# Kernel tuning notes

Measured on AMD Instinct MI355X. Metric: run time of the kernel, lower is better.

The kernel has to match this reference:

```python
import jax, jax.numpy as jnp
import numpy as np

N = 100000
E = 3200000
NFEAT = 256
NHID = 128
NCLASS = 16
TEXT_CNT = 50000


def setup_inputs() -> dict:
    key = jax.random.key(0)
    ks = jax.random.split(key, 12)
    x = jax.random.normal(ks[0], (N, NFEAT), dtype=jnp.float32)
    adj_rows = jax.random.randint(ks[1], (E,), 0, N, dtype=jnp.int32)
    adj_cols = jax.random.randint(ks[2], (E,), 0, N, dtype=jnp.int32)
    # positive normalized-adjacency-like weights (~1/avg_degree scale)
    adj_vals = jax.random.uniform(ks[3], (E,), dtype=jnp.float32) / 32.0
    W1 = jax.random.normal(ks[4], (NFEAT, NHID), dtype=jnp.float32) / np.sqrt(NFEAT)
    b1 = jax.random.normal(ks[5], (NHID,), dtype=jnp.float32) * 0.01
    W2 = jax.random.normal(ks[6], (NHID, NFEAT), dtype=jnp.float32) / np.sqrt(NHID)
    b2 = jax.random.normal(ks[7], (NFEAT,), dtype=jnp.float32) * 0.01
    cW1 = jax.random.normal(ks[8], (NFEAT, NCLASS), dtype=jnp.float32) / np.sqrt(NFEAT)
    cb1 = jax.random.normal(ks[9], (NCLASS,), dtype=jnp.float32) * 0.01
    cW2 = jax.random.normal(ks[10], (NFEAT, NCLASS), dtype=jnp.float32) / np.sqrt(NFEAT)
    cb2 = jax.random.normal(ks[11], (NCLASS,), dtype=jnp.float32) * 0.01
    return {"x": x, "adj_rows": adj_rows, "adj_cols": adj_cols, "adj_vals": adj_vals,
            "W1": W1, "b1": b1, "W2": W2, "b2": b2,
            "cW1": cW1, "cb1": cb1, "cW2": cw2 if (cw2 := None) else cW2, "cb2": cb2}


def spmm(rows, cols, vals, dense):
    # out[r] = sum_{e: rows[e]==r} vals[e] * dense[cols[e]]   (COO SpMM)
    gathered = vals[:, None] * dense[cols]  # [E, D]
    return jax.ops.segment_sum(gathered, rows, num_segments=N)


def reference(x, adj_rows, adj_cols, adj_vals, W1, b1, W2, b2, cW1, cb1, cW2, cb2):
    # gc1: adj @ (x @ W1) + b1, then ReLU (dropout is identity at inference)
    h = jax.nn.relu(spmm(adj_rows, adj_cols, adj_vals, x @ W1) + b1)  # [N, NHID]
    # gc2: adj @ (h @ W2) + b2
    out = spmm(adj_rows, adj_cols, adj_vals, h @ W2) + b2  # [N, NFEAT]
    text_cls = out[:TEXT_CNT] @ cW1 + cb1  # [TEXT_CNT, NCLASS]
    img_cls = out[TEXT_CNT:] @ cW2 + cb2   # [N-TEXT_CNT, NCLASS]
    return (out, text_cls, img_cls)
```

## Files before the change

kernel.cpp:

```cpp
#include <hip/hip_runtime.h>

#define N_NODES  100000
#define N_EDGES  3200000
#define NFEAT    256
#define NHID     128
#define NCLASS   16
#define TEXT_CNT 50000

#define RPB      256
#define NB       ((N_NODES + RPB - 1) / RPB)
#define CAP      16384
#define S_EPT    8
#define NBLKS    ((N_EDGES + 256 * S_EPT - 1) / (256 * S_EPT))

typedef unsigned int uint;
typedef __bf16 bf16x8 __attribute__((ext_vector_type(8)));
typedef __bf16 bf16x4 __attribute__((ext_vector_type(4)));
typedef float f32x4 __attribute__((ext_vector_type(4)));

__device__ inline uint bf16_rne(float f) {
  uint u = __float_as_uint(f);
  return (u + 0x7fffu + ((u >> 16) & 1u)) >> 16;
}
__device__ inline float bf_lo(uint u) { return __uint_as_float(u << 16); }
__device__ inline float bf_hi(uint u) { return __uint_as_float(u & 0xffff0000u); }


__global__ __launch_bounds__(256) void prep_kernel(const float* __restrict__ W1,
                                                   const float* __restrict__ W2,
                                                   const float* __restrict__ b2,
                                                   const float* __restrict__ cW1,
                                                   const float* __restrict__ cb1,
                                                   const float* __restrict__ cW2,
                                                   const float* __restrict__ cb2,
                                                   unsigned short* __restrict__ W1t,
                                                   unsigned short* __restrict__ W2t,
                                                   float* __restrict__ Wc1, float* __restrict__ bc1,
                                                   float* __restrict__ Wc2, float* __restrict__ bc2,
                                                   int* __restrict__ gcursor) {
  int idx = blockIdx.x * 256 + threadIdx.x;
  if (idx < 32768) {
    int n = idx >> 8, k = idx & 255;
    W1t[idx] = (unsigned short)bf16_rne(W1[(size_t)k * NHID + n]);
  } else if (idx < 65536) {
    int i2 = idx - 32768;
    int n = i2 >> 7, k = i2 & 127;
    W2t[i2] = (unsigned short)bf16_rne(W2[(size_t)k * NFEAT + n]);
  } else if (idx < 69632) {
    int e = idx - 65536;
    int set = e >> 11;
    int e2 = e & 2047;
    int i = e2 >> 4, c = e2 & 15;
    const float* cw = set ? cW2 : cW1;
    float acc = 0.f;
    for (int k = 0; k < NFEAT; ++k)
      acc += W2[(size_t)i * NFEAT + k] * cw[k * NCLASS + c];
    (set ? Wc2 : Wc1)[e2] = acc;
    if (e < 32) {
      int s2 = e >> 4, c2 = e & 15;
      const float* cwb = s2 ? cW2 : cW1;
      float b = (s2 ? cb2 : cb1)[c2];
      for (int k = 0; k < NFEAT; ++k) b += b2[k] * cwb[k * NCLASS + c2];
      (s2 ? bc2 : bc1)[c2] = b;
    }
  } else if (idx < 69632 + NB) {
    int b = idx - 69632;
    gcursor[b] = b * CAP;
  }
}


__device__ __forceinline__ void scatter_body(int bx, const int* __restrict__ rows,
                                             const int* __restrict__ cols,
                                             const float* __restrict__ vals,
                                             int* __restrict__ gcursor,
                                             int2* __restrict__ packed, int E) {
  __shared__ int hist[NB];
  __shared__ int cur[NB];
  for (int i = threadIdx.x; i < NB; i += 256) hist[i] = 0;
  __syncthreads();
  int base = bx * (256 * S_EPT);
#pragma unroll
  for (int i = 0; i < S_EPT; ++i) {
    int e = base + i * 256 + threadIdx.x;
    if (e < E) atomicAdd(&hist[rows[e] >> 8], 1);
  }
  __syncthreads();
  for (int i = threadIdx.x; i < NB; i += 256) {
    int h = hist[i];
    cur[i] = h ? atomicAdd(&gcursor[i], h) : 0;
  }
  __syncthreads();
#pragma unroll
  for (int i = 0; i < S_EPT; ++i) {
    int e = base + i * 256 + threadIdx.x;
    if (e < E) {
      int r = rows[e];
      int b = r >> 8;
      int p = atomicAdd(&cur[b], 1);
      if (p < ((b + 1) << 14))
        packed[p] = make_int2(((r & 255) << 17) | cols[e], __float_as_int(vals[e]));
    }
  }
}


template <int A_FP32, int OUT_BF16, int K, int N>
__device__ __forceinline__ void gemm_body(int bx, int by, const void* __restrict__ Aptr,
                                          const __bf16* __restrict__ Bt,
                                          const float* __restrict__ bias,
                                          void* __restrict__ Cptr, int M) {
  __shared__ __bf16 As[128 * 40];
  __shared__ __bf16 Bs[128 * 40];
  int tid = threadIdx.x;
  int lane = tid & 63;
  int w = tid >> 6;
  int wr = w >> 1, wc = w & 1;
  int brow = bx * 128;
  int bcol = by * 128;
  int r16 = lane & 15, kb = lane >> 4;

  f32x4 acc[4][4];
#pragma unroll
  for (int m = 0; m < 4; ++m)
#pragma unroll
    for (int n = 0; n < 4; ++n) acc[m][n] = (f32x4){0.f, 0.f, 0.f, 0.f};

  for (int k0 = 0; k0 < K; k0 += 32) {
    if (A_FP32) {
      const float* A = (const float*)Aptr;
#pragma unroll
      for (int i = 0; i < 4; ++i) {
        int idx = tid + i * 256;
        int row = idx >> 3;
        int kq = (idx & 7) << 2;
        int gr = brow + row;
        float4 v = make_float4(0.f, 0.f, 0.f, 0.f);
        if (gr < M) v = *(const float4*)&A[(size_t)gr * K + k0 + kq];
        bf16x4 o;
        o[0] = (__bf16)v.x; o[1] = (__bf16)v.y; o[2] = (__bf16)v.z; o[3] = (__bf16)v.w;
        *(bf16x4*)&As[row * 40 + kq] = o;
      }
    } else {
      const __bf16* A = (const __bf16*)Aptr;
#pragma unroll
      for (int i = 0; i < 2; ++i) {
        int idx = tid + i * 256;
        int row = idx >> 2;
        int kq = (idx & 3) << 3;
        int gr = brow + row;
        bf16x8 v = {};
        if (gr < M) v = *(const bf16x8*)&A[(size_t)gr * K + k0 + kq];
        *(bf16x8*)&As[row * 40 + kq] = v;
      }
    }
#pragma unroll
    for (int i = 0; i < 2; ++i) {
      int idx = tid + i * 256;
      int col = idx >> 2;
      int kq = (idx & 3) << 3;
      bf16x8 v = *(const bf16x8*)&Bt[(size_t)(bcol + col) * K + k0 + kq];
      *(bf16x8*)&Bs[col * 40 + kq] = v;
    }
    __syncthreads();

    bf16x8 a[4], b[4];
#pragma unroll
    for (int m = 0; m < 4; ++m)
      a[m] = *(bf16x8*)&As[(wr * 64 + m * 16 + r16) * 40 + kb * 8];
#pragma unroll
    for (int n = 0; n < 4; ++n)
      b[n] = *(bf16x8*)&Bs[(wc * 64 + n * 16 + r16) * 40 + kb * 8];
#pragma unroll
    for (int m = 0; m < 4; ++m)
#pragma unroll
      for (int n = 0; n < 4; ++n)
        acc[m][n] = __builtin_amdgcn_mfma_f32_16x16x32_bf16(a[m], b[n], acc[m][n], 0, 0, 0);
    __syncthreads();
  }

  int crow0 = brow + wr * 64;
  int ccol0 = bcol + wc * 64;
#pragma unroll
  for (int n = 0; n < 4; ++n) {
    int col = ccol0 + n * 16 + r16;
    float bv = bias ? bias[col] : 0.f;
#pragma unroll
    for (int m = 0; m < 4; ++m) {
#pragma unroll
      for (int r = 0; r < 4; ++r) {
        int row = crow0 + m * 16 + kb * 4 + r;
        if (row < M) {
          float val = acc[m][n][r] + bv;
          if (OUT_BF16)
            ((unsigned short*)Cptr)[(size_t)row * N + col] = (unsigned short)bf16_rne(val);
          else
            ((float*)Cptr)[(size_t)row * N + col] = val;
        }
      }
    }
  }
}


__global__ __launch_bounds__(256) void fused_scatter_gemm1_kernel(
    const int* __restrict__ rows, const int* __restrict__ cols, const float* __restrict__ vals,
    int* __restrict__ gcursor, int2* __restrict__ packedA, int E,
    const float* __restrict__ x, const __bf16* __restrict__ W1t, uint* __restrict__ t1u, int M) {
  if (blockIdx.x < NBLKS)
    scatter_body(blockIdx.x, rows, cols, vals, gcursor, packedA, E);
  else
    gemm_body<1, 1, NFEAT, NHID>(blockIdx.x - NBLKS, 0, x, W1t, nullptr, t1u, M);
}


__global__ __launch_bounds__(512) void bucket_scan_kernel(const int* __restrict__ gcursor,
                                                          int* __restrict__ bbase) {
  __shared__ int s[512];
  int t = threadIdx.x;
  int v = (t < NB) ? (gcursor[t] - t * CAP) : 0;
  s[t] = v;
  __syncthreads();
  for (int off = 1; off < 512; off <<= 1) {
    int u = (t >= off) ? s[t - off] : 0;
    __syncthreads();
    s[t] += u;
    __syncthreads();
  }
  if (t < NB) bbase[t] = s[t] - v;
  if (t == 0) bbase[NB] = N_EDGES;
}


__global__ __launch_bounds__(512) void csr_finalize_kernel(const int* __restrict__ bbase,
                                                           const int2* __restrict__ packed_in,
                                                           int2* __restrict__ packed_out,
                                                           int* __restrict__ row_ptr) {
  __shared__ int hist[RPB];
  __shared__ int cur[RPB];
  int b = blockIdx.x;
  int s0 = b * CAP;
  int gout = bbase[b];
  int cnt = bbase[b + 1] - gout;
  int end = s0 + cnt;
  int t = threadIdx.x;
  if (t < RPB) hist[t] = 0;
  __syncthreads();
  {
    int i = s0 + t;
    for (; i + 1536 < end; i += 2048) {
      int2 a0 = packed_in[i], a1 = packed_in[i + 512];
      int2 a2 = packed_in[i + 1024], a3 = packed_in[i + 1536];
      atomicAdd(&hist[a0.x >> 17], 1);
      atomicAdd(&hist[a1.x >> 17], 1);
      atomicAdd(&hist[a2.x >> 17], 1);
      atomicAdd(&hist[a3.x >> 17], 1);
    }
    for (; i < end; i += 512) atomicAdd(&hist[packed_in[i].x >> 17], 1);
  }
  __syncthreads();
  int v = (t < RPB) ? hist[t] : 0;
  if (t < RPB) cur[t] = v;
  __syncthreads();
  for (int off = 1; off < RPB; off <<= 1) {
    int u = (t >= off && t < RPB) ? cur[t - off] : 0;
    __syncthreads();
    if (t < RPB) cur[t] += u;
    __syncthreads();
  }
  if (t < RPB) {
    int rbase = gout + cur[t] - v;
    int row = b * RPB + t;
    if (row < N_NODES) row_ptr[row] = rbase;
    cur[t] = rbase;
  }
  if (b == 0 && t == 0) row_ptr[N_NODES] = N_EDGES;
  __syncthreads();
  {
    int i = s0 + t;
    for (; i + 1536 < end; i += 2048) {
      int2 a0 = packed_in[i], a1 = packed_in[i + 512];
      int2 a2 = packed_in[i + 1024], a3 = packed_in[i + 1536];
      int p0 = atomicAdd(&cur[a0.x >> 17], 1);
      int p1 = atomicAdd(&cur[a1.x >> 17], 1);
      int p2 = atomicAdd(&cur[a2.x >> 17], 1);
      int p3 = atomicAdd(&cur[a3.x >> 17], 1);
      packed_out[p0] = make_int2((a0.x & 0x1FFFF) << 8, a0.y);
      packed_out[p1] = make_int2((a1.x & 0x1FFFF) << 8, a1.y);
      packed_out[p2] = make_int2((a2.x & 0x1FFFF) << 8, a2.y);
      packed_out[p3] = make_int2((a3.x & 0x1FFFF) << 8, a3.y);
    }
    for (; i < end; i += 512) {
      int2 pk = packed_in[i];
      int p = atomicAdd(&cur[pk.x >> 17], 1);
      packed_out[p] = make_int2((pk.x & 0x1FFFF) << 8, pk.y);
    }
  }
}


__global__ __launch_bounds__(256) void spmm_bf16_kernel(const int* __restrict__ row_ptr,
                                                        const int2* __restrict__ packed,
                                                        const uint* __restrict__ src,
                                                        uint* __restrict__ dst,
                                                        const float* __restrict__ bias,
                                                        int relu, int nrows) {
  int tid = threadIdx.x;
  int lane = tid & 63;
  int half = lane >> 5;
  int l32 = lane & 31;
  int row = blockIdx.x * 4 + (tid >> 6);
  if (row >= nrows) return;
  int s = row_ptr[row];
  int e = row_ptr[row + 1];
  const char* srcb = (const char*)src + (l32 << 3);
  float a0 = 0.f, a1 = 0.f, a2 = 0.f, a3 = 0.f;
  int i = s;
  for (; i + 16 <= e; i += 16) {
    int2 m0 = packed[i + 0 + half], m1 = packed[i + 2 + half];
    int2 m2 = packed[i + 4 + half], m3 = packed[i + 6 + half];
    int2 m4 = packed[i + 8 + half], m5 = packed[i + 10 + half];
    int2 m6 = packed[i + 12 + half], m7 = packed[i + 14 + half];
    uint2 u0 = *(const uint2*)(srcb + (uint)m0.x);
    uint2 u1 = *(const uint2*)(srcb + (uint)m1.x);
    uint2 u2 = *(const uint2*)(srcb + (uint)m2.x);
    uint2 u3 = *(const uint2*)(srcb + (uint)m3.x);
    uint2 u4 = *(const uint2*)(srcb + (uint)m4.x);
    uint2 u5 = *(const uint2*)(srcb + (uint)m5.x);
    uint2 u6 = *(const uint2*)(srcb + (uint)m6.x);
    uint2 u7 = *(const uint2*)(srcb + (uint)m7.x);
    float v0 = __int_as_float(m0.y), v1 = __int_as_float(m1.y);
    float v2 = __int_as_float(m2.y), v3 = __int_as_float(m3.y);
    float v4 = __int_as_float(m4.y), v5 = __int_as_float(m5.y);
    float v6 = __int_as_float(m6.y), v7 = __int_as_float(m7.y);
    a0 += v0 * bf_lo(u0.x); a1 += v0 * bf_hi(u0.x); a2 += v0 * bf_lo(u0.y); a3 += v0 * bf_hi(u0.y);
    a0 += v1 * bf_lo(u1.x); a1 += v1 * bf_hi(u1.x); a2 += v1 * bf_lo(u1.y); a3 += v1 * bf_hi(u1.y);
    a0 += v2 * bf_lo(u2.x); a1 += v2 * bf_hi(u2.x); a2 += v2 * bf_lo(u2.y); a3 += v2 * bf_hi(u2.y);
    a0 += v3 * bf_lo(u3.x); a1 += v3 * bf_hi(u3.x); a2 += v3 * bf_lo(u3.y); a3 += v3 * bf_hi(u3.y);
    a0 += v4 * bf_lo(u4.x); a1 += v4 * bf_hi(u4.x); a2 += v4 * bf_lo(u4.y); a3 += v4 * bf_hi(u4.y);
    a0 += v5 * bf_lo(u5.x); a1 += v5 * bf_hi(u5.x); a2 += v5 * bf_lo(u5.y); a3 += v5 * bf_hi(u5.y);
    a0 += v6 * bf_lo(u6.x); a1 += v6 * bf_hi(u6.x); a2 += v6 * bf_lo(u6.y); a3 += v6 * bf_hi(u6.y);
    a0 += v7 * bf_lo(u7.x); a1 += v7 * bf_hi(u7.x); a2 += v7 * bf_lo(u7.y); a3 += v7 * bf_hi(u7.y);
  }
  for (; i + 8 <= e; i += 8) {
    int2 m0 = packed[i + 0 + half], m1 = packed[i + 2 + half];
    int2 m2 = packed[i + 4 + half], m3 = packed[i + 6 + half];
    uint2 u0 = *(const uint2*)(srcb + (uint)m0.x);
    uint2 u1 = *(const uint2*)(srcb + (uint)m1.x);
    uint2 u2 = *(const uint2*)(srcb + (uint)m2.x);
    uint2 u3 = *(const uint2*)(srcb + (uint)m3.x);
    float v0 = __int_as_float(m0.y), v1 = __int_as_float(m1.y);
    float v2 = __int_as_float(m2.y), v3 = __int_as_float(m3.y);
    a0 += v0 * bf_lo(u0.x); a1 += v0 * bf_hi(u0.x); a2 += v0 * bf_lo(u0.y); a3 += v0 * bf_hi(u0.y);
    a0 += v1 * bf_lo(u1.x); a1 += v1 * bf_hi(u1.x); a2 += v1 * bf_lo(u1.y); a3 += v1 * bf_hi(u1.y);
    a0 += v2 * bf_lo(u2.x); a1 += v2 * bf_hi(u2.x); a2 += v2 * bf_lo(u2.y); a3 += v2 * bf_hi(u2.y);
    a0 += v3 * bf_lo(u3.x); a1 += v3 * bf_hi(u3.x); a2 += v3 * bf_lo(u3.y); a3 += v3 * bf_hi(u3.y);
  }
  for (; i + 4 <= e; i += 4) {
    int2 m0 = packed[i + 0 + half], m1 = packed[i + 2 + half];
    uint2 u0 = *(const uint2*)(srcb + (uint)m0.x);
    uint2 u1 = *(const uint2*)(srcb + (uint)m1.x);
    float v0 = __int_as_float(m0.y), v1 = __int_as_float(m1.y);
    a0 += v0 * bf_lo(u0.x); a1 += v0 * bf_hi(u0.x); a2 += v0 * bf_lo(u0.y); a3 += v0 * bf_hi(u0.y);
    a0 += v1 * bf_lo(u1.x); a1 += v1 * bf_hi(u1.x); a2 += v1 * bf_lo(u1.y); a3 += v1 * bf_hi(u1.y);
  }
  for (; i < e; i += 2) {
    int ee = i + half;
    int ok = ee < e;
    int2 m = packed[ok ? ee : (e - 1)];
    uint2 u = *(const uint2*)(srcb + (uint)m.x);
    float v = ok ? __int_as_float(m.y) : 0.f;
    a0 += v * bf_lo(u.x); a1 += v * bf_hi(u.x); a2 += v * bf_lo(u.y); a3 += v * bf_hi(u.y);
  }
  a0 += __shfl_xor(a0, 32); a1 += __shfl_xor(a1, 32);
  a2 += __shfl_xor(a2, 32); a3 += __shfl_xor(a3, 32);
  if (half == 0) {
    if (bias) {
      a0 += bias[4 * l32 + 0]; a1 += bias[4 * l32 + 1];
      a2 += bias[4 * l32 + 2]; a3 += bias[4 * l32 + 3];
    }
    if (relu) {
      a0 = fmaxf(a0, 0.f); a1 = fmaxf(a1, 0.f);
      a2 = fmaxf(a2, 0.f); a3 = fmaxf(a3, 0.f);
    }
    uint2 o;
    o.x = bf16_rne(a0) | (bf16_rne(a1) << 16);
    o.y = bf16_rne(a2) | (bf16_rne(a3) << 16);
    *(uint2*)&dst[(size_t)row * 64 + l32 * 2] = o;
  }
}


template <int A_FP32, int OUT_BF16, int K, int N>
__global__ __launch_bounds__(256) void gemm_mfma_kernel(const void* __restrict__ Aptr,
                                                        const __bf16* __restrict__ Bt,
                                                        const float* __restrict__ bias,
                                                        void* __restrict__ Cptr, int M) {
  gemm_body<A_FP32, OUT_BF16, K, N>(blockIdx.x, blockIdx.y, Aptr, Bt, bias, Cptr, M);
}


__global__ __launch_bounds__(256) void cls_kernel(const uint* __restrict__ t3,
                                                  const float* __restrict__ Wc1,
                                                  const float* __restrict__ bc1,
                                                  const float* __restrict__ Wc2,
                                                  const float* __restrict__ bc2,
                                                  float* __restrict__ out1,
                                                  float* __restrict__ out2) {
  int half = gridDim.x >> 1;
  int region = blockIdx.x >= half;
  int bid = region ? blockIdx.x - half : blockIdx.x;
  const float* Wc = region ? Wc2 : Wc1;
  const float* bc = region ? bc2 : bc1;
  float* outp = region ? out2 : out1;
  int row0 = region ? TEXT_CNT : 0;
  int nrows = region ? (N_NODES - TEXT_CNT) : TEXT_CNT;

  int lane = threadIdx.x & 63;
  int wav = bid * 4 + (threadIdx.x >> 6);
  int nw = half * 4;
  int c = lane & 15;
  int kg = lane >> 4;
  float w[32];
#pragma unroll
  for (int j = 0; j < 32; ++j) w[j] = Wc[(kg * 32 + j) * NCLASS + c];
  float bcv = bc[c];
  for (int r = wav; r < nrows; r += nw) {
    const uint4* rp = (const uint4*)&t3[(size_t)(row0 + r) * 64 + kg * 16];
    float acc = 0.f;
#pragma unroll
    for (int q = 0; q < 4; ++q) {
      uint4 u = rp[q];
      acc += bf_lo(u.x) * w[q * 8 + 0] + bf_hi(u.x) * w[q * 8 + 1]
           + bf_lo(u.y) * w[q * 8 + 2] + bf_hi(u.y) * w[q * 8 + 3]
           + bf_lo(u.z) * w[q * 8 + 4] + bf_hi(u.z) * w[q * 8 + 5]
           + bf_lo(u.w) * w[q * 8 + 6] + bf_hi(u.w) * w[q * 8 + 7];
    }
    acc += __shfl_xor(acc, 16);
    acc += __shfl_xor(acc, 32);
    if (lane < 16) outp[(size_t)r * NCLASS + lane] = acc + bcv;
  }
}


extern "C" void kernel_launch(void* const* d_in, const int* in_sizes, int n_in,
                              void* d_out, int out_size, void* d_ws, size_t ws_size,
                              hipStream_t stream) {
  const float* x     = (const float*)d_in[0];
  const int*   arows = (const int*)d_in[1];
  const int*   acols = (const int*)d_in[2];
  const float* avals = (const float*)d_in[3];
  const float* W1    = (const float*)d_in[4];
  const float* b1    = (const float*)d_in[5];
  const float* W2    = (const float*)d_in[6];
  const float* b2    = (const float*)d_in[7];
  const float* cW1   = (const float*)d_in[8];
  const float* cb1   = (const float*)d_in[9];
  const float* cW2   = (const float*)d_in[10];
  const float* cb2   = (const float*)d_in[11];
  float* outp = (float*)d_out;

  char* ws = (char*)d_ws;
  size_t off = 0;
  auto alloc = [&](size_t bytes) -> void* {
    void* p = ws + off;
    off += (bytes + 255) & ~(size_t)255;
    return p;
  };
  uint*  t1u     = (uint*) alloc((size_t)N_NODES * 64 * 4);
  uint*  hu      = (uint*) alloc((size_t)N_NODES * 64 * 4);
  uint*  t3u     = (uint*) alloc((size_t)N_NODES * 64 * 4);
  int2*  packedA = (int2*) alloc((size_t)NB * CAP * 8);
  int2*  packedB = (int2*) alloc((size_t)N_EDGES * 8);
  int*   bbase   = (int*)  alloc((size_t)(NB + 1) * 4);
  int*   gcursor = (int*)  alloc((size_t)NB * 4);
  int*   rowp    = (int*)  alloc((size_t)(N_NODES + 1) * 4);
  unsigned short* W1t = (unsigned short*)alloc((size_t)NHID * NFEAT * 2);
  unsigned short* W2t = (unsigned short*)alloc((size_t)NFEAT * NHID * 2);
  float* Wc1     = (float*)alloc(NHID * NCLASS * 4);
  float* Wc2     = (float*)alloc(NHID * NCLASS * 4);
  float* bc1     = (float*)alloc(64);
  float* bc2     = (float*)alloc(64);

  prep_kernel<<<(69632 + NB + 255) / 256, 256, 0, stream>>>(
      W1, W2, b2, cW1, cb1, cW2, cb2, W1t, W2t, Wc1, bc1, Wc2, bc2, gcursor);

  int mblk = (N_NODES + 127) / 128;
  fused_scatter_gemm1_kernel<<<NBLKS + mblk, 256, 0, stream>>>(
      arows, acols, avals, gcursor, packedA, N_EDGES,
      x, (const __bf16*)W1t, t1u, N_NODES);

  bucket_scan_kernel<<<1, 512, 0, stream>>>(gcursor, bbase);
  csr_finalize_kernel<<<NB, 512, 0, stream>>>(bbase, packedA, packedB, rowp);

  spmm_bf16_kernel<<<(N_NODES + 3) / 4, 256, 0, stream>>>(rowp, packedB, t1u, hu, b1, 1, N_NODES);
  spmm_bf16_kernel<<<(N_NODES + 3) / 4, 256, 0, stream>>>(rowp, packedB, hu, t3u, nullptr, 0, N_NODES);
  gemm_mfma_kernel<0, 0, NHID, NFEAT><<<dim3(mblk, 2), 256, 0, stream>>>(
      t3u, (const __bf16*)W2t, b2, outp, N_NODES);
  cls_kernel<<<2048, 256, 0, stream>>>(t3u, Wc1, bc1, Wc2, bc2,
      outp + (size_t)N_NODES * NFEAT,
      outp + (size_t)N_NODES * NFEAT + (size_t)TEXT_CNT * NCLASS);
}
```

Before: 465.3 us.

## Unfuse scatter from GEMM1, add nontemporal streaming loads, enlarge scatter per-thread work

Splits the fused scatter+GEMM1 kernel back into a standalone bucket scatter kernel and a separate GEMM1 launch that runs after CSR finalize. The scatter now handles 32 edges per thread instead of 8, and streaming reads of edge arrays, packed COO/CSR entries, x, and the final fp32 output store switch to nontemporal loads and stores. The aim is to keep the reused feature tables cached during the gathers and to cut atomic traffic on the global cursors. The cost is that the scatter no longer overlaps with GEMM1, there is one more launch, and fewer scatter blocks means less parallelism.

```diff
diff --git a/kernel.cpp b/kernel.cpp
--- a/kernel.cpp
+++ b/kernel.cpp
@@ -10,13 +10,14 @@
 #define RPB      256
 #define NB       ((N_NODES + RPB - 1) / RPB)
 #define CAP      16384
-#define S_EPT    8
+#define S_EPT    32
 #define NBLKS    ((N_EDGES + 256 * S_EPT - 1) / (256 * S_EPT))
 
 typedef unsigned int uint;
 typedef __bf16 bf16x8 __attribute__((ext_vector_type(8)));
 typedef __bf16 bf16x4 __attribute__((ext_vector_type(4)));
 typedef float f32x4 __attribute__((ext_vector_type(4)));
+typedef int i32x2 __attribute__((ext_vector_type(2)));
 
 __device__ inline uint bf16_rne(float f) {
   uint u = __float_as_uint(f);
@@ -70,20 +71,20 @@
 }
 
 
-__device__ __forceinline__ void scatter_body(int bx, const int* __restrict__ rows,
-                                             const int* __restrict__ cols,
-                                             const float* __restrict__ vals,
-                                             int* __restrict__ gcursor,
-                                             int2* __restrict__ packed, int E) {
+__global__ __launch_bounds__(256) void bucket_scatter_kernel(const int* __restrict__ rows,
+                                                             const int* __restrict__ cols,
+                                                             const float* __restrict__ vals,
+                                                             int* __restrict__ gcursor,
+                                                             int2* __restrict__ packed, int E) {
   __shared__ int hist[NB];
   __shared__ int cur[NB];
   for (int i = threadIdx.x; i < NB; i += 256) hist[i] = 0;
   __syncthreads();
-  int base = bx * (256 * S_EPT);
+  int base = blockIdx.x * (256 * S_EPT);
 #pragma unroll
   for (int i = 0; i < S_EPT; ++i) {
     int e = base + i * 256 + threadIdx.x;
-    if (e < E) atomicAdd(&hist[rows[e] >> 8], 1);
+    if (e < E) atomicAdd(&hist[__builtin_nontemporal_load(&rows[e]) >> 8], 1);
   }
   __syncthreads();
   for (int i = threadIdx.x; i < NB; i += 256) {
@@ -95,122 +96,15 @@
   for (int i = 0; i < S_EPT; ++i) {
     int e = base + i * 256 + threadIdx.x;
     if (e < E) {
-      int r = rows[e];
+      int r = __builtin_nontemporal_load(&rows[e]);
+      int c = __builtin_nontemporal_load(&cols[e]);
+      float v = __builtin_nontemporal_load(&vals[e]);
       int b = r >> 8;
       int p = atomicAdd(&cur[b], 1);
       if (p < ((b + 1) << 14))
-        packed[p] = make_int2(((r & 255) << 17) | cols[e], __float_as_int(vals[e]));
-    }
-  }
-}
-
-
-template <int A_FP32, int OUT_BF16, int K, int N>
-__device__ __forceinline__ void gemm_body(int bx, int by, const void* __restrict__ Aptr,
-                                          const __bf16* __restrict__ Bt,
-                                          const float* __restrict__ bias,
-                                          void* __restrict__ Cptr, int M) {
-  __shared__ __bf16 As[128 * 40];
-  __shared__ __bf16 Bs[128 * 40];
-  int tid = threadIdx.x;
-  int lane = tid & 63;
-  int w = tid >> 6;
-  int wr = w >> 1, wc = w & 1;
-  int brow = bx * 128;
-  int bcol = by * 128;
-  int r16 = lane & 15, kb = lane >> 4;
-
-  f32x4 acc[4][4];
-#pragma unroll
-  for (int m = 0; m < 4; ++m)
-#pragma unroll
-    for (int n = 0; n < 4; ++n) acc[m][n] = (f32x4){0.f, 0.f, 0.f, 0.f};
-
-  for (int k0 = 0; k0 < K; k0 += 32) {
-    if (A_FP32) {
-      const float* A = (const float*)Aptr;
-#pragma unroll
-      for (int i = 0; i < 4; ++i) {
-        int idx = tid + i * 256;
-        int row = idx >> 3;
-        int kq = (idx & 7) << 2;
-        int gr = brow + row;
-        float4 v = make_float4(0.f, 0.f, 0.f, 0.f);
-        if (gr < M) v = *(const float4*)&A[(size_t)gr * K + k0 + kq];
-        bf16x4 o;
-        o[0] = (__bf16)v.x; o[1] = (__bf16)v.y; o[2] = (__bf16)v.z; o[3] = (__bf16)v.w;
-        *(bf16x4*)&As[row * 40 + kq] = o;
-      }
-    } else {
-      const __bf16* A = (const __bf16*)Aptr;
-#pragma unroll
-      for (int i = 0; i < 2; ++i) {
-        int idx = tid + i * 256;
-        int row = idx >> 2;
-        int kq = (idx & 3) << 3;
-        int gr = brow + row;
-        bf16x8 v = {};
-        if (gr < M) v = *(const bf16x8*)&A[(size_t)gr * K + k0 + kq];
-        *(bf16x8*)&As[row * 40 + kq] = v;
-      }
-    }
-#pragma unroll
-    for (int i = 0; i < 2; ++i) {
-      int idx = tid + i * 256;
-      int col = idx >> 2;
-      int kq = (idx & 3) << 3;
-      bf16x8 v = *(const bf16x8*)&Bt[(size_t)(bcol + col) * K + k0 + kq];
-      *(bf16x8*)&Bs[col * 40 + kq] = v;
-    }
-    __syncthreads();
-
-    bf16x8 a[4], b[4];
-#pragma unroll
-    for (int m = 0; m < 4; ++m)
-      a[m] = *(bf16x8*)&As[(wr * 64 + m * 16 + r16) * 40 + kb * 8];
-#pragma unroll
-    for (int n = 0; n < 4; ++n)
-      b[n] = *(bf16x8*)&Bs[(wc * 64 + n * 16 + r16) * 40 + kb * 8];
-#pragma unroll
-    for (int m = 0; m < 4; ++m)
-#pragma unroll
-      for (int n = 0; n < 4; ++n)
-        acc[m][n] = __builtin_amdgcn_mfma_f32_16x16x32_bf16(a[m], b[n], acc[m][n], 0, 0, 0);
-    __syncthreads();
-  }
-
-  int crow0 = brow + wr * 64;
-  int ccol0 = bcol + wc * 64;
-#pragma unroll
-  for (int n = 0; n < 4; ++n) {
-    int col = ccol0 + n * 16 + r16;
-    float bv = bias ? bias[col] : 0.f;
-#pragma unroll
-    for (int m = 0; m < 4; ++m) {
-#pragma unroll
-      for (int r = 0; r < 4; ++r) {
-        int row = crow0 + m * 16 + kb * 4 + r;
-        if (row < M) {
-          float val = acc[m][n][r] + bv;
-          if (OUT_BF16)
-            ((unsigned short*)Cptr)[(size_t)row * N + col] = (unsigned short)bf16_rne(val);
-          else
-            ((float*)Cptr)[(size_t)row * N + col] = val;
-        }
-      }
-    }
-  }
-}
-
-
-__global__ __launch_bounds__(256) void fused_scatter_gemm1_kernel(
-    const int* __restrict__ rows, const int* __restrict__ cols, const float* __restrict__ vals,
-    int* __restrict__ gcursor, int2* __restrict__ packedA, int E,
-    const float* __restrict__ x, const __bf16* __restrict__ W1t, uint* __restrict__ t1u, int M) {
-  if (blockIdx.x < NBLKS)
-    scatter_body(blockIdx.x, rows, cols, vals, gcursor, packedA, E);
-  else
-    gemm_body<1, 1, NFEAT, NHID>(blockIdx.x - NBLKS, 0, x, W1t, nullptr, t1u, M);
+        packed[p] = make_int2(((r & 255) << 17) | c, __float_as_int(v));
+    }
+  }
 }
 
 
@@ -244,19 +138,22 @@
   int cnt = bbase[b + 1] - gout;
   int end = s0 + cnt;
   int t = threadIdx.x;
+  const i32x2* pin = (const i32x2*)packed_in;
   if (t < RPB) hist[t] = 0;
   __syncthreads();
   {
     int i = s0 + t;
     for (; i + 1536 < end; i += 2048) {
-      int2 a0 = packed_in[i], a1 = packed_in[i + 512];
-      int2 a2 = packed_in[i + 1024], a3 = packed_in[i + 1536];
+      i32x2 a0 = __builtin_nontemporal_load(&pin[i]);
+      i32x2 a1 = __builtin_nontemporal_load(&pin[i + 512]);
+      i32x2 a2 = __builtin_nontemporal_load(&pin[i + 1024]);
+      i32x2 a3 = __builtin_nontemporal_load(&pin[i + 1536]);
       atomicAdd(&hist[a0.x >> 17], 1);
       atomicAdd(&hist[a1.x >> 17], 1);
       atomicAdd(&hist[a2.x >> 17], 1);
       atomicAdd(&hist[a3.x >> 17], 1);
     }
-    for (; i < end; i += 512) atomicAdd(&hist[packed_in[i].x >> 17], 1);
+    for (; i < end; i += 512) atomicAdd(&hist[__builtin_nontemporal_load(&pin[i]).x >> 17], 1);
   }
   __syncthreads();
   int v = (t < RPB) ? hist[t] : 0;
@@ -279,8 +176,10 @@
   {
     int i = s0 + t;
     for (; i + 1536 < end; i += 2048) {
-      int2 a0 = packed_in[i], a1 = packed_in[i + 512];
-      int2 a2 = packed_in[i + 1024], a3 = packed_in[i + 1536];
+      i32x2 a0 = __builtin_nontemporal_load(&pin[i]);
+      i32x2 a1 = __builtin_nontemporal_load(&pin[i + 512]);
+      i32x2 a2 = __builtin_nontemporal_load(&pin[i + 1024]);
+      i32x2 a3 = __builtin_nontemporal_load(&pin[i + 1536]);
       int p0 = atomicAdd(&cur[a0.x >> 17], 1);
       int p1 = atomicAdd(&cur[a1.x >> 17], 1);
       int p2 = atomicAdd(&cur[a2.x >> 17], 1);
@@ -291,7 +190,7 @@
       packed_out[p3] = make_int2((a3.x & 0x1FFFF) << 8, a3.y);
     }
     for (; i < end; i += 512) {
-      int2 pk = packed_in[i];
+      i32x2 pk = __builtin_nontemporal_load(&pin[i]);
       int p = atomicAdd(&cur[pk.x >> 17], 1);
       packed_out[p] = make_int2((pk.x & 0x1FFFF) << 8, pk.y);
     }
@@ -314,13 +213,18 @@
   int s = row_ptr[row];
   int e = row_ptr[row + 1];
   const char* srcb = (const char*)src + (l32 << 3);
+  const i32x2* pk = (const i32x2*)packed;
   float a0 = 0.f, a1 = 0.f, a2 = 0.f, a3 = 0.f;
   int i = s;
   for (; i + 16 <= e; i += 16) {
-    int2 m0 = packed[i + 0 + half], m1 = packed[i + 2 + half];
-    int2 m2 = packed[i + 4 + half], m3 = packed[i + 6 + half];
-    int2 m4 = packed[i + 8 + half], m5 = packed[i + 10 + half];
-    int2 m6 = packed[i + 12 + half], m7 = packed[i + 14 + half];
+    i32x2 m0 = __builtin_nontemporal_load(&pk[i + 0 + half]);
+    i32x2 m1 = __builtin_nontemporal_load(&pk[i + 2 + half]);
+    i32x2 m2 = __builtin_nontemporal_load(&pk[i + 4 + half]);
+    i32x2 m3 = __builtin_nontemporal_load(&pk[i + 6 + half]);
+    i32x2 m4 = __builtin_nontemporal_load(&pk[i + 8 + half]);
+    i32x2 m5 = __builtin_nontemporal_load(&pk[i + 10 + half]);
+    i32x2 m6 = __builtin_nontemporal_load(&pk[i + 12 + half]);
+    i32x2 m7 = __builtin_nontemporal_load(&pk[i + 14 + half]);
     uint2 u0 = *(const uint2*)(srcb + (uint)m0.x);
     uint2 u1 = *(const uint2*)(srcb + (uint)m1.x);
     uint2 u2 = *(const uint2*)(srcb + (uint)m2.x);
@@ -343,8 +247,10 @@
     a0 += v7 * bf_lo(u7.x); a1 += v7 * bf_hi(u7.x); a2 += v7 * bf_lo(u7.y); a3 += v7 * bf_hi(u7.y);
   }
   for (; i + 8 <= e; i += 8) {
-    int2 m0 = packed[i + 0 + half], m1 = packed[i + 2 + half];
-    int2 m2 = packed[i + 4 + half], m3 = packed[i + 6 + half];
+    i32x2 m0 = __builtin_nontemporal_load(&pk[i + 0 + half]);
+    i32x2 m1 = __builtin_nontemporal_load(&pk[i + 2 + half]);
+    i32x2 m2 = __builtin_nontemporal_load(&pk[i + 4 + half]);
+    i32x2 m3 = __builtin_nontemporal_load(&pk[i + 6 + half]);
     uint2 u0 = *(const uint2*)(srcb + (uint)m0.x);
     uint2 u1 = *(const uint2*)(srcb + (uint)m1.x);
     uint2 u2 = *(const uint2*)(srcb + (uint)m2.x);
@@ -357,7 +263,8 @@
     a0 += v3 * bf_lo(u3.x); a1 += v3 * bf_hi(u3.x); a2 += v3 * bf_lo(u3.y); a3 += v3 * bf_hi(u3.y);
   }
   for (; i + 4 <= e; i += 4) {
-    int2 m0 = packed[i + 0 + half], m1 = packed[i + 2 + half];
+    i32x2 m0 = __builtin_nontemporal_load(&pk[i + 0 + half]);
+    i32x2 m1 = __builtin_nontemporal_load(&pk[i + 2 + half]);
     uint2 u0 = *(const uint2*)(srcb + (uint)m0.x);
     uint2 u1 = *(const uint2*)(srcb + (uint)m1.x);
     float v0 = __int_as_float(m0.y), v1 = __int_as_float(m1.y);
@@ -367,7 +274,7 @@
   for (; i < e; i += 2) {
     int ee = i + half;
     int ok = ee < e;
-    int2 m = packed[ok ? ee : (e - 1)];
+    i32x2 m = pk[ok ? ee : (e - 1)];
     uint2 u = *(const uint2*)(srcb + (uint)m.x);
     float v = ok ? __int_as_float(m.y) : 0.f;
     a0 += v * bf_lo(u.x); a1 += v * bf_hi(u.x); a2 += v * bf_lo(u.y); a3 += v * bf_hi(u.y);
@@ -396,7 +303,96 @@
                                                         const __bf16* __restrict__ Bt,
                                                         const float* __restrict__ bias,
                                                         void* __restrict__ Cptr, int M) {
-  gemm_body<A_FP32, OUT_BF16, K, N>(blockIdx.x, blockIdx.y, Aptr, Bt, bias, Cptr, M);
+  __shared__ __bf16 As[128 * 40];
+  __shared__ __bf16 Bs[128 * 40];
+  int tid = threadIdx.x;
+  int lane = tid & 63;
+  int w = tid >> 6;
+  int wr = w >> 1, wc = w & 1;
+  int brow = blockIdx.x * 128;
+  int bcol = blockIdx.y * 128;
+  int r16 = lane & 15, kb = lane >> 4;
+
+  f32x4 acc[4][4];
+#pragma unroll
+  for (int m = 0; m < 4; ++m)
+#pragma unroll
+    for (int n = 0; n < 4; ++n) acc[m][n] = (f32x4){0.f, 0.f, 0.f, 0.f};
+
+  for (int k0 = 0; k0 < K; k0 += 32) {
+    if (A_FP32) {
+      const float* A = (const float*)Aptr;
+#pragma unroll
+      for (int i = 0; i < 4; ++i) {
+        int idx = tid + i * 256;
+        int row = idx >> 3;
+        int kq = (idx & 7) << 2;
+        int gr = brow + row;
+        f32x4 v = (f32x4){0.f, 0.f, 0.f, 0.f};
+        if (gr < M) v = __builtin_nontemporal_load((const f32x4*)&A[(size_t)gr * K + k0 + kq]);
+        bf16x4 o;
+        o[0] = (__bf16)v[0]; o[1] = (__bf16)v[1]; o[2] = (__bf16)v[2]; o[3] = (__bf16)v[3];
+        *(bf16x4*)&As[row * 40 + kq] = o;
+      }
+    } else {
+      const __bf16* A = (const __bf16*)Aptr;
+#pragma unroll
+      for (int i = 0; i < 2; ++i) {
+        int idx = tid + i * 256;
+        int row = idx >> 2;
+        int kq = (idx & 3) << 3;
+        int gr = brow + row;
+        bf16x8 v = {};
+        if (gr < M) v = *(const bf16x8*)&A[(size_t)gr * K + k0 + kq];
+        *(bf16x8*)&As[row * 40 + kq] = v;
+      }
+    }
+#pragma unroll
+    for (int i = 0; i < 2; ++i) {
+      int idx = tid + i * 256;
+      int col = idx >> 2;
+      int kq = (idx & 3) << 3;
+      bf16x8 v = *(const bf16x8*)&Bt[(size_t)(bcol + col) * K + k0 + kq];
+      *(bf16x8*)&Bs[col * 40 + kq] = v;
+    }
+    __syncthreads();
+
+    bf16x8 a[4], b[4];
+#pragma unroll
+    for (int m = 0; m < 4; ++m)
+      a[m] = *(bf16x8*)&As[(wr * 64 + m * 16 + r16) * 40 + kb * 8];
+#pragma unroll
+    for (int n = 0; n < 4; ++n)
+      b[n] = *(bf16x8*)&Bs[(wc * 64 + n * 16 + r16) * 40 + kb * 8];
+#pragma unroll
+    for (int m = 0; m < 4; ++m)
+#pragma unroll
+      for (int n = 0; n < 4; ++n)
+        acc[m][n] = __builtin_amdgcn_mfma_f32_16x16x32_bf16(a[m], b[n], acc[m][n], 0, 0, 0);
+    __syncthreads();
+  }
+
+  int crow0 = brow + wr * 64;
+  int ccol0 = bcol + wc * 64;
+#pragma unroll
+  for (int n = 0; n < 4; ++n) {
+    int col = ccol0 + n * 16 + r16;
+    float bv = bias ? bias[col] : 0.f;
+#pragma unroll
+    for (int m = 0; m < 4; ++m) {
+#pragma unroll
+      for (int r = 0; r < 4; ++r) {
+        int row = crow0 + m * 16 + kb * 4 + r;
+        if (row < M) {
+          float val = acc[m][n][r] + bv;
+          if (OUT_BF16)
+            ((unsigned short*)Cptr)[(size_t)row * N + col] = (unsigned short)bf16_rne(val);
+          else
+            __builtin_nontemporal_store(val, &((float*)Cptr)[(size_t)row * N + col]);
+        }
+      }
+    }
+  }
 }
 
 
@@ -485,14 +481,14 @@
   prep_kernel<<<(69632 + NB + 255) / 256, 256, 0, stream>>>(
       W1, W2, b2, cW1, cb1, cW2, cb2, W1t, W2t, Wc1, bc1, Wc2, bc2, gcursor);
 
-  int mblk = (N_NODES + 127) / 128;
-  fused_scatter_gemm1_kernel<<<NBLKS + mblk, 256, 0, stream>>>(
-      arows, acols, avals, gcursor, packedA, N_EDGES,
-      x, (const __bf16*)W1t, t1u, N_NODES);
+  bucket_scatter_kernel<<<NBLKS, 256, 0, stream>>>(arows, acols, avals, gcursor, packedA, N_EDGES);
 
   bucket_scan_kernel<<<1, 512, 0, stream>>>(gcursor, bbase);
   csr_finalize_kernel<<<NB, 512, 0, stream>>>(bbase, packedA, packedB, rowp);
 
+  int mblk = (N_NODES + 127) / 128;
+  gemm_mfma_kernel<1, 1, NFEAT, NHID><<<dim3(mblk, 1), 256, 0, stream>>>(
+      x, (const __bf16*)W1t, nullptr, t1u, N_NODES);
   spmm_bf16_kernel<<<(N_NODES + 3) / 4, 256, 0, stream>>>(rowp, packedB, t1u, hu, b1, 1, N_NODES);
   spmm_bf16_kernel<<<(N_NODES + 3) / 4, 256, 0, stream>>>(rowp, packedB, hu, t3u, nullptr, 0, N_NODES);
   gemm_mfma_kernel<0, 0, NHID, NFEAT><<<dim3(mblk, 2), 256, 0, stream>>>(
```

New measurement: 512.6 us. 1.1x slower.

## Unfuse scatter from GEMM1 and quadruple edges per scatter block

Applied to the files above, without the earlier changes.

Splits the fused scatter+GEMM1 kernel back into a standalone bucket scatter kernel and a separate GEMM1 launch placed after CSR finalize. Each scatter block now handles 32 edges per thread instead of 8, which cuts the number of blocks and the per-block global cursor atomics and histogram clears. In exchange it loses the overlap of scatter with the x@W1 GEMM, adds a launch, and lowers scatter parallelism.

```diff
diff --git a/kernel.cpp b/kernel.cpp
--- a/kernel.cpp
+++ b/kernel.cpp
@@ -10,7 +10,7 @@
 #define RPB      256
 #define NB       ((N_NODES + RPB - 1) / RPB)
 #define CAP      16384
-#define S_EPT    8
+#define S_EPT    32
 #define NBLKS    ((N_EDGES + 256 * S_EPT - 1) / (256 * S_EPT))
 
 typedef unsigned int uint;
@@ -70,16 +70,16 @@
 }
 
 
-__device__ __forceinline__ void scatter_body(int bx, const int* __restrict__ rows,
-                                             const int* __restrict__ cols,
-                                             const float* __restrict__ vals,
-                                             int* __restrict__ gcursor,
-                                             int2* __restrict__ packed, int E) {
+__global__ __launch_bounds__(256) void bucket_scatter_kernel(const int* __restrict__ rows,
+                                                             const int* __restrict__ cols,
+                                                             const float* __restrict__ vals,
+                                                             int* __restrict__ gcursor,
+                                                             int2* __restrict__ packed, int E) {
   __shared__ int hist[NB];
   __shared__ int cur[NB];
   for (int i = threadIdx.x; i < NB; i += 256) hist[i] = 0;
   __syncthreads();
-  int base = bx * (256 * S_EPT);
+  int base = blockIdx.x * (256 * S_EPT);
 #pragma unroll
   for (int i = 0; i < S_EPT; ++i) {
     int e = base + i * 256 + threadIdx.x;
@@ -102,115 +102,6 @@
         packed[p] = make_int2(((r & 255) << 17) | cols[e], __float_as_int(vals[e]));
     }
   }
-}
-
-
-template <int A_FP32, int OUT_BF16, int K, int N>
-__device__ __forceinline__ void gemm_body(int bx, int by, const void* __restrict__ Aptr,
-                                          const __bf16* __restrict__ Bt,
-                                          const float* __restrict__ bias,
-                                          void* __restrict__ Cptr, int M) {
-  __shared__ __bf16 As[128 * 40];
-  __shared__ __bf16 Bs[128 * 40];
-  int tid = threadIdx.x;
-  int lane = tid & 63;
-  int w = tid >> 6;
-  int wr = w >> 1, wc = w & 1;
-  int brow = bx * 128;
-  int bcol = by * 128;
-  int r16 = lane & 15, kb = lane >> 4;
-
-  f32x4 acc[4][4];
-#pragma unroll
-  for (int m = 0; m < 4; ++m)
-#pragma unroll
-    for (int n = 0; n < 4; ++n) acc[m][n] = (f32x4){0.f, 0.f, 0.f, 0.f};
-
-  for (int k0 = 0; k0 < K; k0 += 32) {
-    if (A_FP32) {
-      const float* A = (const float*)Aptr;
-#pragma unroll
-      for (int i = 0; i < 4; ++i) {
-        int idx = tid + i * 256;
-        int row = idx >> 3;
-        int kq = (idx & 7) << 2;
-        int gr = brow + row;
-        float4 v = make_float4(0.f, 0.f, 0.f, 0.f);
-        if (gr < M) v = *(const float4*)&A[(size_t)gr * K + k0 + kq];
-        bf16x4 o;
-        o[0] = (__bf16)v.x; o[1] = (__bf16)v.y; o[2] = (__bf16)v.z; o[3] = (__bf16)v.w;
-        *(bf16x4*)&As[row * 40 + kq] = o;
-      }
-    } else {
-      const __bf16* A = (const __bf16*)Aptr;
-#pragma unroll
-      for (int i = 0; i < 2; ++i) {
-        int idx = tid + i * 256;
-        int row = idx >> 2;
-        int kq = (idx & 3) << 3;
-        int gr = brow + row;
-        bf16x8 v = {};
-        if (gr < M) v = *(const bf16x8*)&A[(size_t)gr * K + k0 + kq];
-        *(bf16x8*)&As[row * 40 + kq] = v;
-      }
-    }
-#pragma unroll
-    for (int i = 0; i < 2; ++i) {
-      int idx = tid + i * 256;
-      int col = idx >> 2;
-      int kq = (idx & 3) << 3;
-      bf16x8 v = *(const bf16x8*)&Bt[(size_t)(bcol + col) * K + k0 + kq];
-      *(bf16x8*)&Bs[col * 40 + kq] = v;
-    }
-    __syncthreads();
-
-    bf16x8 a[4], b[4];
-#pragma unroll
-    for (int m = 0; m < 4; ++m)
-      a[m] = *(bf16x8*)&As[(wr * 64 + m * 16 + r16) * 40 + kb * 8];
-#pragma unroll
-    for (int n = 0; n < 4; ++n)
-      b[n] = *(bf16x8*)&Bs[(wc * 64 + n * 16 + r16) * 40 + kb * 8];
-#pragma unroll
-    for (int m = 0; m < 4; ++m)
-#pragma unroll
-      for (int n = 0; n < 4; ++n)
-        acc[m][n] = __builtin_amdgcn_mfma_f32_16x16x32_bf16(a[m], b[n], acc[m][n], 0, 0, 0);
-    __syncthreads();
-  }
-
-  int crow0 = brow + wr * 64;
-  int ccol0 = bcol + wc * 64;
-#pragma unroll
-  for (int n = 0; n < 4; ++n) {
-    int col = ccol0 + n * 16 + r16;
-    float bv = bias ? bias[col] : 0.f;
-#pragma unroll
-    for (int m = 0; m < 4; ++m) {
-#pragma unroll
-      for (int r = 0; r < 4; ++r) {
-        int row = crow0 + m * 16 + kb * 4 + r;
-        if (row < M) {
-          float val = acc[m][n][r] + bv;
-          if (OUT_BF16)
-            ((unsigned short*)Cptr)[(size_t)row * N + col] = (unsigned short)bf16_rne(val);
-          else
-            ((float*)Cptr)[(size_t)row * N + col] = val;
-        }
-      }
-    }
-  }
-}
-
-
-__global__ __launch_bounds__(256) void fused_scatter_gemm1_kernel(
-    const int* __restrict__ rows, const int* __restrict__ cols, const float* __restrict__ vals,
-    int* __restrict__ gcursor, int2* __restrict__ packedA, int E,
-    const float* __restrict__ x, const __bf16* __restrict__ W1t, uint* __restrict__ t1u, int M) {
-  if (blockIdx.x < NBLKS)
-    scatter_body(blockIdx.x, rows, cols, vals, gcursor, packedA, E);
-  else
-    gemm_body<1, 1, NFEAT, NHID>(blockIdx.x - NBLKS, 0, x, W1t, nullptr, t1u, M);
 }
 
 
@@ -396,7 +287,96 @@
                                                         const __bf16* __restrict__ Bt,
                                                         const float* __restrict__ bias,
                                                         void* __restrict__ Cptr, int M) {
-  gemm_body<A_FP32, OUT_BF16, K, N>(blockIdx.x, blockIdx.y, Aptr, Bt, bias, Cptr, M);
+  __shared__ __bf16 As[128 * 40];
+  __shared__ __bf16 Bs[128 * 40];
+  int tid = threadIdx.x;
+  int lane = tid & 63;
+  int w = tid >> 6;
+  int wr = w >> 1, wc = w & 1;
+  int brow = blockIdx.x * 128;
+  int bcol = blockIdx.y * 128;
+  int r16 = lane & 15, kb = lane >> 4;
+
+  f32x4 acc[4][4];
+#pragma unroll
+  for (int m = 0; m < 4; ++m)
+#pragma unroll
+    for (int n = 0; n < 4; ++n) acc[m][n] = (f32x4){0.f, 0.f, 0.f, 0.f};
+
+  for (int k0 = 0; k0 < K; k0 += 32) {
+    if (A_FP32) {
+      const float* A = (const float*)Aptr;
+#pragma unroll
+      for (int i = 0; i < 4; ++i) {
+        int idx = tid + i * 256;
+        int row = idx >> 3;
+        int kq = (idx & 7) << 2;
+        int gr = brow + row;
+        float4 v = make_float4(0.f, 0.f, 0.f, 0.f);
+        if (gr < M) v = *(const float4*)&A[(size_t)gr * K + k0 + kq];
+        bf16x4 o;
+        o[0] = (__bf16)v.x; o[1] = (__bf16)v.y; o[2] = (__bf16)v.z; o[3] = (__bf16)v.w;
+        *(bf16x4*)&As[row * 40 + kq] = o;
+      }
+    } else {
+      const __bf16* A = (const __bf16*)Aptr;
+#pragma unroll
+      for (int i = 0; i < 2; ++i) {
+        int idx = tid + i * 256;
+        int row = idx >> 2;
+        int kq = (idx & 3) << 3;
+        int gr = brow + row;
+        bf16x8 v = {};
+        if (gr < M) v = *(const bf16x8*)&A[(size_t)gr * K + k0 + kq];
+        *(bf16x8*)&As[row * 40 + kq] = v;
+      }
+    }
+#pragma unroll
+    for (int i = 0; i < 2; ++i) {
+      int idx = tid + i * 256;
+      int col = idx >> 2;
+      int kq = (idx & 3) << 3;
+      bf16x8 v = *(const bf16x8*)&Bt[(size_t)(bcol + col) * K + k0 + kq];
+      *(bf16x8*)&Bs[col * 40 + kq] = v;
+    }
+    __syncthreads();
+
+    bf16x8 a[4], b[4];
+#pragma unroll
+    for (int m = 0; m < 4; ++m)
+      a[m] = *(bf16x8*)&As[(wr * 64 + m * 16 + r16) * 40 + kb * 8];
+#pragma unroll
+    for (int n = 0; n < 4; ++n)
+      b[n] = *(bf16x8*)&Bs[(wc * 64 + n * 16 + r16) * 40 + kb * 8];
+#pragma unroll
+    for (int m = 0; m < 4; ++m)
+#pragma unroll
+      for (int n = 0; n < 4; ++n)
+        acc[m][n] = __builtin_amdgcn_mfma_f32_16x16x32_bf16(a[m], b[n], acc[m][n], 0, 0, 0);
+    __syncthreads();
+  }
+
+  int crow0 = brow + wr * 64;
+  int ccol0 = bcol + wc * 64;
+#pragma unroll
+  for (int n = 0; n < 4; ++n) {
+    int col = ccol0 + n * 16 + r16;
+    float bv = bias ? bias[col] : 0.f;
+#pragma unroll
+    for (int m = 0; m < 4; ++m) {
+#pragma unroll
+      for (int r = 0; r < 4; ++r) {
+        int row = crow0 + m * 16 + kb * 4 + r;
+        if (row < M) {
+          float val = acc[m][n][r] + bv;
+          if (OUT_BF16)
+            ((unsigned short*)Cptr)[(size_t)row * N + col] = (unsigned short)bf16_rne(val);
+          else
+            ((float*)Cptr)[(size_t)row * N + col] = val;
+        }
+      }
+    }
+  }
 }
 
 
@@ -485,14 +465,14 @@
   prep_kernel<<<(69632 + NB + 255) / 256, 256, 0, stream>>>(
       W1, W2, b2, cW1, cb1, cW2, cb2, W1t, W2t, Wc1, bc1, Wc2, bc2, gcursor);
 
-  int mblk = (N_NODES + 127) / 128;
-  fused_scatter_gemm1_kernel<<<NBLKS + mblk, 256, 0, stream>>>(
-      arows, acols, avals, gcursor, packedA, N_EDGES,
-      x, (const __bf16*)W1t, t1u, N_NODES);
+  bucket_scatter_kernel<<<NBLKS, 256, 0, stream>>>(arows, acols, avals, gcursor, packedA, N_EDGES);
 
   bucket_scan_kernel<<<1, 512, 0, stream>>>(gcursor, bbase);
   csr_finalize_kernel<<<NB, 512, 0, stream>>>(bbase, packedA, packedB, rowp);
 
+  int mblk = (N_NODES + 127) / 128;
+  gemm_mfma_kernel<1, 1, NFEAT, NHID><<<dim3(mblk, 1), 256, 0, stream>>>(
+      x, (const __bf16*)W1t, nullptr, t1u, N_NODES);
   spmm_bf16_kernel<<<(N_NODES + 3) / 4, 256, 0, stream>>>(rowp, packedB, t1u, hu, b1, 1, N_NODES);
   spmm_bf16_kernel<<<(N_NODES + 3) / 4, 256, 0, stream>>>(rowp, packedB, hu, t3u, nullptr, 0, N_NODES);
   gemm_mfma_kernel<0, 0, NHID, NFEAT><<<dim3(mblk, 2), 256, 0, stream>>>(
```

After: 478.9 us. +2.9%, slower.

## Fold bucket scan into CSR finalize and share LDS in fused scatter/GEMM kernel

Applied to the files above, without the earlier changes.

Removes the single-block bucket_scan kernel by having every csr_finalize block recompute the 391-entry prefix scan over gcursor itself, which saves one launch and one serialized tiny kernel. The scatter and GEMM paths of the fused kernel now share one dynamic shared-memory buffer instead of separate static allocations, cutting per-block LDS so occupancy can rise. Scatter edges per thread go from 8 to 32, giving fewer blocks and fewer global cursor atomics but less parallelism. The redundant per-block scan adds some sync-heavy work to every finalize block.

```diff
diff --git a/kernel.cpp b/kernel.cpp
--- a/kernel.cpp
+++ b/kernel.cpp
@@ -10,8 +10,9 @@
 #define RPB      256
 #define NB       ((N_NODES + RPB - 1) / RPB)
 #define CAP      16384
-#define S_EPT    8
+#define S_EPT    32
 #define NBLKS    ((N_EDGES + 256 * S_EPT - 1) / (256 * S_EPT))
+#define GEMM_LDS (2 * 128 * 40 * 2)
 
 typedef unsigned int uint;
 typedef __bf16 bf16x8 __attribute__((ext_vector_type(8)));
@@ -74,9 +75,10 @@
                                              const int* __restrict__ cols,
                                              const float* __restrict__ vals,
                                              int* __restrict__ gcursor,
-                                             int2* __restrict__ packed, int E) {
-  __shared__ int hist[NB];
-  __shared__ int cur[NB];
+                                             int2* __restrict__ packed, int E,
+                                             int* __restrict__ smem) {
+  int* hist = smem;
+  int* cur = smem + NB;
   for (int i = threadIdx.x; i < NB; i += 256) hist[i] = 0;
   __syncthreads();
   int base = bx * (256 * S_EPT);
@@ -109,9 +111,8 @@
 __device__ __forceinline__ void gemm_body(int bx, int by, const void* __restrict__ Aptr,
                                           const __bf16* __restrict__ Bt,
                                           const float* __restrict__ bias,
-                                          void* __restrict__ Cptr, int M) {
-  __shared__ __bf16 As[128 * 40];
-  __shared__ __bf16 Bs[128 * 40];
+                                          void* __restrict__ Cptr, int M,
+                                          __bf16* __restrict__ As, __bf16* __restrict__ Bs) {
   int tid = threadIdx.x;
   int lane = tid & 63;
   int w = tid >> 6;
@@ -203,47 +204,41 @@
 }
 
 
-__global__ __launch_bounds__(256) void fused_scatter_gemm1_kernel(
+__global__ __launch_bounds__(256) void fused_sg1_kernel(
     const int* __restrict__ rows, const int* __restrict__ cols, const float* __restrict__ vals,
     int* __restrict__ gcursor, int2* __restrict__ packedA, int E,
     const float* __restrict__ x, const __bf16* __restrict__ W1t, uint* __restrict__ t1u, int M) {
+  extern __shared__ __align__(16) char dynbuf[];
   if (blockIdx.x < NBLKS)
-    scatter_body(blockIdx.x, rows, cols, vals, gcursor, packedA, E);
+    scatter_body(blockIdx.x, rows, cols, vals, gcursor, packedA, E, (int*)dynbuf);
   else
-    gemm_body<1, 1, NFEAT, NHID>(blockIdx.x - NBLKS, 0, x, W1t, nullptr, t1u, M);
-}
-
-
-__global__ __launch_bounds__(512) void bucket_scan_kernel(const int* __restrict__ gcursor,
-                                                          int* __restrict__ bbase) {
-  __shared__ int s[512];
-  int t = threadIdx.x;
-  int v = (t < NB) ? (gcursor[t] - t * CAP) : 0;
-  s[t] = v;
-  __syncthreads();
-  for (int off = 1; off < 512; off <<= 1) {
-    int u = (t >= off) ? s[t - off] : 0;
-    __syncthreads();
-    s[t] += u;
-    __syncthreads();
-  }
-  if (t < NB) bbase[t] = s[t] - v;
-  if (t == 0) bbase[NB] = N_EDGES;
-}
-
-
-__global__ __launch_bounds__(512) void csr_finalize_kernel(const int* __restrict__ bbase,
+    gemm_body<1, 1, NFEAT, NHID>(blockIdx.x - NBLKS, 0, x, W1t, nullptr, t1u, M,
+                                 (__bf16*)dynbuf, (__bf16*)dynbuf + 128 * 40);
+}
+
+
+__global__ __launch_bounds__(512) void csr_finalize_kernel(const int* __restrict__ gcursor,
                                                            const int2* __restrict__ packed_in,
                                                            int2* __restrict__ packed_out,
                                                            int* __restrict__ row_ptr) {
+  __shared__ int pre[512];
   __shared__ int hist[RPB];
   __shared__ int cur[RPB];
   int b = blockIdx.x;
+  int t = threadIdx.x;
+  int cntt = (t < NB) ? (gcursor[t] - t * CAP) : 0;
+  pre[t] = cntt;
+  __syncthreads();
+  for (int off = 1; off < 512; off <<= 1) {
+    int u = (t >= off) ? pre[t - off] : 0;
+    __syncthreads();
+    pre[t] += u;
+    __syncthreads();
+  }
+  int cnt = gcursor[b] - b * CAP;
+  int gout = pre[b] - cnt;
   int s0 = b * CAP;
-  int gout = bbase[b];
-  int cnt = bbase[b + 1] - gout;
   int end = s0 + cnt;
-  int t = threadIdx.x;
   if (t < RPB) hist[t] = 0;
   __syncthreads();
   {
@@ -396,7 +391,9 @@
                                                         const __bf16* __restrict__ Bt,
                                                         const float* __restrict__ bias,
                                                         void* __restrict__ Cptr, int M) {
-  gemm_body<A_FP32, OUT_BF16, K, N>(blockIdx.x, blockIdx.y, Aptr, Bt, bias, Cptr, M);
+  __shared__ __align__(16) __bf16 smem[2 * 128 * 40];
+  gemm_body<A_FP32, OUT_BF16, K, N>(blockIdx.x, blockIdx.y, Aptr, Bt, bias, Cptr, M,
+                                    smem, smem + 128 * 40);
 }
 
 
@@ -472,7 +469,6 @@
   uint*  t3u     = (uint*) alloc((size_t)N_NODES * 64 * 4);
   int2*  packedA = (int2*) alloc((size_t)NB * CAP * 8);
   int2*  packedB = (int2*) alloc((size_t)N_EDGES * 8);
-  int*   bbase   = (int*)  alloc((size_t)(NB + 1) * 4);
   int*   gcursor = (int*)  alloc((size_t)NB * 4);
   int*   rowp    = (int*)  alloc((size_t)(N_NODES + 1) * 4);
   unsigned short* W1t = (unsigned short*)alloc((size_t)NHID * NFEAT * 2);
@@ -486,12 +482,11 @@
       W1, W2, b2, cW1, cb1, cW2, cb2, W1t, W2t, Wc1, bc1, Wc2, bc2, gcursor);
 
   int mblk = (N_NODES + 127) / 128;
-  fused_scatter_gemm1_kernel<<<NBLKS + mblk, 256, 0, stream>>>(
+  fused_sg1_kernel<<<NBLKS + mblk, 256, GEMM_LDS, stream>>>(
       arows, acols, avals, gcursor, packedA, N_EDGES,
       x, (const __bf16*)W1t, t1u, N_NODES);
 
-  bucket_scan_kernel<<<1, 512, 0, stream>>>(gcursor, bbase);
-  csr_finalize_kernel<<<NB, 512, 0, stream>>>(bbase, packedA, packedB, rowp);
+  csr_finalize_kernel<<<NB, 512, 0, stream>>>(gcursor, packedA, packedB, rowp);
 
   spmm_bf16_kernel<<<(N_NODES + 3) / 4, 256, 0, stream>>>(rowp, packedB, t1u, hu, b1, 1, N_NODES);
   spmm_bf16_kernel<<<(N_NODES + 3) / 4, 256, 0, stream>>>(rowp, packedB, hu, t3u, nullptr, 0, N_NODES);
```

Measured after the change: 445.2 us. -4.3%, faster.
